# Kernel optimization log

Measured on AMD Instinct MI355X. Metric: run time of the kernel, lower is better.

## Reference

```python
import jax, jax.numpy as jnp
import numpy as np

N_NODES = 100000
N_FEATURES = 512
N_HIDDEN = 256
N_EDGES = 3200000


def setup_inputs() -> dict:
    key = jax.random.key(0)
    k_x, k_r, k_c, k_v, k_w, k_b = jax.random.split(key, 6)
    x = jax.random.normal(k_x, (1, N_NODES, N_FEATURES), dtype=jnp.float32)
    adj_rows = jax.random.randint(k_r, (N_EDGES,), 0, N_NODES, dtype=jnp.int32)
    adj_cols = jax.random.randint(k_c, (N_EDGES,), 0, N_NODES, dtype=jnp.int32)
    adj_vals = jax.random.uniform(k_v, (N_EDGES,), dtype=jnp.float32)
    # Linear params: xavier_normal_ on weight [H, F], default bias init
    std = float(np.sqrt(2.0 / (N_FEATURES + N_HIDDEN)))
    W = jax.random.normal(k_w, (N_HIDDEN, N_FEATURES), dtype=jnp.float32) * std
    bound = float(1.0 / np.sqrt(N_FEATURES))
    b = jax.random.uniform(k_b, (N_HIDDEN,), dtype=jnp.float32, minval=-bound, maxval=bound)
    alpha = jnp.asarray(0.25, dtype=jnp.float32)  # PReLU default single-param init
    return {"x": x, "adj_rows": adj_rows, "adj_cols": adj_cols,
            "adj_vals": adj_vals, "W": W, "b": b, "alpha": alpha}


def reference(x, adj_rows, adj_cols, adj_vals, W, b, alpha):
    # Linear: [1, N, F] @ [F, H] + [H] -> squeeze to [N, H]
    h = (jnp.einsum('bnf,hf->bnh', x, W) + b)[0]
    # spmm(adj, h): gather source rows, scale by edge value, scatter-add to dest rows
    msgs = adj_vals[:, None] * h[adj_cols]              # [E, H]
    agg = jax.ops.segment_sum(msgs, adj_rows, num_segments=N_NODES)  # [N, H]
    out = jnp.where(agg >= 0, agg, alpha * agg)         # PReLU
    return out[None]                                     # [1, N, H]
```

## Files before the change

### kernel.cpp

```cpp
#include <hip/hip_runtime.h>


#define K_DIM 512
#define H_DIM 256

#define BIN_ROWS 512
#define NBIN_MAX 256
#define EB 18432
#define P1_CHUNK 4096
#define P1_PER_T 4
#define SPU 8

typedef __attribute__((ext_vector_type(8))) short short8;
typedef __attribute__((ext_vector_type(4))) float floatx4;

__device__ inline short f32_to_bf16(float f) {
    unsigned u = __float_as_uint(f);
    u += 0x7fffu + ((u >> 16) & 1u);
    return (short)(u >> 16);
}
__device__ inline float bf16_to_f32(unsigned short u) {
    return __uint_as_float(((unsigned)u) << 16);
}

__global__ __launch_bounds__(256) void convert_w_kernel(
    const float* __restrict__ W, unsigned short* __restrict__ Wbf)
{
    int i = (blockIdx.x * 256 + threadIdx.x) * 8;
    float4 a = *(const float4*)(W + i);
    float4 b = *(const float4*)(W + i + 4);
    short8 v;
    v[0] = f32_to_bf16(a.x); v[1] = f32_to_bf16(a.y);
    v[2] = f32_to_bf16(a.z); v[3] = f32_to_bf16(a.w);
    v[4] = f32_to_bf16(b.x); v[5] = f32_to_bf16(b.y);
    v[6] = f32_to_bf16(b.z); v[7] = f32_to_bf16(b.w);
    *(short8*)((short*)Wbf + i) = v;
}

#define GT_M 128
#define GT_N 256
#define GT_K 32
#define LDSW 32

__global__ __launch_bounds__(256, 2) void gemm_bf16_kernel(
    const float* __restrict__ A,
    const unsigned short* __restrict__ Wbf,
    const float* __restrict__ bias,
    unsigned short* __restrict__ H,
    int M)
{
    __shared__ short As[GT_M * LDSW];
    __shared__ short Bs[GT_N * LDSW];

    const int tid  = threadIdx.x;
    const int m0   = blockIdx.x * GT_M;

    const int wave = tid >> 6;
    const int lane = tid & 63;
    const int wm   = (wave & 1) * 64;
    const int wn   = (wave >> 1) * 128;
    const int quad = lane >> 4;
    const int l16  = lane & 15;

    const int srow  = tid >> 1;
    const int shalf = tid & 1;

    floatx4 acc[4][8] = {};

    for (int k0 = 0; k0 < K_DIM; k0 += GT_K) {
        {
            int gm = m0 + srow;
            float f[16];
            if (gm < M) {
                const float* src = A + (size_t)gm * K_DIM + k0 + shalf * 16;
                *(float4*)(f + 0)  = *(const float4*)(src + 0);
                *(float4*)(f + 4)  = *(const float4*)(src + 4);
                *(float4*)(f + 8)  = *(const float4*)(src + 8);
                *(float4*)(f + 12) = *(const float4*)(src + 12);
            } else {
                #pragma unroll
                for (int j = 0; j < 16; ++j) f[j] = 0.f;
            }
            short8 v0, v1;
            #pragma unroll
            for (int j = 0; j < 8; ++j) { v0[j] = f32_to_bf16(f[j]); v1[j] = f32_to_bf16(f[8 + j]); }
            *(short8*)&As[srow * LDSW + shalf * 16 + 0] = v0;
            *(short8*)&As[srow * LDSW + shalf * 16 + 8] = v1;
        }
        #pragma unroll
        for (int it = 0; it < 2; ++it) {
            int gn = srow + it * 128;
            const unsigned short* src = Wbf + (size_t)gn * K_DIM + k0 + shalf * 16;
            short8 v0 = *(const short8*)(src + 0);
            short8 v1 = *(const short8*)(src + 8);
            *(short8*)&Bs[gn * LDSW + shalf * 16 + 0] = v0;
            *(short8*)&Bs[gn * LDSW + shalf * 16 + 8] = v1;
        }
        __syncthreads();

        short8 af[4], bf[8];
        #pragma unroll
        for (int t = 0; t < 4; ++t)
            af[t] = *(const short8*)&As[(wm + t * 16 + l16) * LDSW + quad * 8];
        #pragma unroll
        for (int t = 0; t < 8; ++t)
            bf[t] = *(const short8*)&Bs[(wn + t * 16 + l16) * LDSW + quad * 8];
        #pragma unroll
        for (int i = 0; i < 4; ++i)
            #pragma unroll
            for (int j = 0; j < 8; ++j)
                acc[i][j] = __builtin_amdgcn_mfma_f32_16x16x32_bf16(af[i], bf[j], acc[i][j], 0, 0, 0);
        __syncthreads();
    }

    #pragma unroll
    for (int j = 0; j < 8; ++j) {
        int gcol = wn + j * 16 + l16;
        float bj = bias[gcol];
        #pragma unroll
        for (int i = 0; i < 4; ++i) {
            int rbase = m0 + wm + i * 16 + quad * 4;
            #pragma unroll
            for (int r = 0; r < 4; ++r) {
                int gm = rbase + r;
                if (gm < M)
                    H[(size_t)gm * H_DIM + gcol] =
                        (unsigned short)f32_to_bf16(acc[i][j][r] + bj);
            }
        }
    }
}

__global__ __launch_bounds__(1024) void partition_kernel(
    const int* __restrict__ rows, const int* __restrict__ cols,
    const float* __restrict__ vals, int* __restrict__ binCursor,
    int2* __restrict__ binned, int E, int nbins)
{
    __shared__ int hist[NBIN_MAX];
    __shared__ int binOff[NBIN_MAX];
    __shared__ int gbase[NBIN_MAX];
    __shared__ int cursor[NBIN_MAX];
    __shared__ int sc[2][NBIN_MAX];
    __shared__ int2 stage[P1_CHUNK];
    __shared__ unsigned char binOf[P1_CHUNK];

    const int tid = threadIdx.x;
    const int e0  = blockIdx.x * P1_CHUNK;
    const int total = min(P1_CHUNK, E - e0);

    int r[P1_PER_T], c[P1_PER_T];
    float v[P1_PER_T];
    #pragma unroll
    for (int i = 0; i < P1_PER_T; ++i) {
        int e = e0 + tid + i * 1024;
        if (e < E) { r[i] = rows[e]; c[i] = cols[e]; v[i] = vals[e]; }
        else       { r[i] = -1; c[i] = 0; v[i] = 0.f; }
    }

    if (tid < NBIN_MAX) hist[tid] = 0;
    __syncthreads();
    #pragma unroll
    for (int i = 0; i < P1_PER_T; ++i)
        if (r[i] >= 0) atomicAdd(&hist[r[i] >> 9], 1);
    __syncthreads();

    if (tid < NBIN_MAX) sc[0][tid] = hist[tid];
    __syncthreads();
    int cur = 0;
    for (int d = 1; d < NBIN_MAX; d <<= 1) {
        if (tid < NBIN_MAX) {
            int y = sc[cur][tid];
            if (tid >= d) y += sc[cur][tid - d];
            sc[cur ^ 1][tid] = y;
        }
        __syncthreads();
        cur ^= 1;
    }
    if (tid < NBIN_MAX) {
        int x    = hist[tid];
        int excl = sc[cur][tid] - x;
        binOff[tid] = excl;
        cursor[tid] = excl;
        if (tid < nbins) gbase[tid] = atomicAdd(&binCursor[tid], x);
        else             gbase[tid] = 0;
    }
    __syncthreads();

    #pragma unroll
    for (int i = 0; i < P1_PER_T; ++i) {
        if (r[i] >= 0) {
            int bin  = r[i] >> 9;
            int lpos = atomicAdd(&cursor[bin], 1);
            stage[lpos] = make_int2(((r[i] & (BIN_ROWS - 1)) << 17) | c[i],
                                    __float_as_int(v[i]));
            binOf[lpos] = (unsigned char)bin;
        }
    }
    __syncthreads();

    #pragma unroll
    for (int i = 0; i < P1_PER_T; ++i) {
        int idx = tid + i * 1024;
        if (idx < total) {
            int bin = binOf[idx];
            int rel = gbase[bin] + (idx - binOff[bin]);
            if (rel < EB)
                binned[(size_t)bin * EB + rel] = stage[idx];
        }
    }
}

__global__ __launch_bounds__(1024) void binsort_kernel(
    const int2* __restrict__ binned, const int* __restrict__ binCursor,
    int2* __restrict__ sorted, int* __restrict__ rowstart,
    int* __restrict__ degArr, int M)
{
    __shared__ int hist[BIN_ROWS];
    __shared__ int cursor[BIN_ROWS];
    __shared__ int sc[2][BIN_ROWS];

    const int b   = blockIdx.x;
    const int tid = threadIdx.x;
    int cnt = binCursor[b]; if (cnt > EB) cnt = EB;
    int rows_here = M - b * BIN_ROWS; if (rows_here > BIN_ROWS) rows_here = BIN_ROWS;

    if (tid < BIN_ROWS) hist[tid] = 0;
    __syncthreads();
    const int2* src = binned + (size_t)b * EB;
    for (int i = tid; i < cnt; i += 1024)
        atomicAdd(&hist[((unsigned)src[i].x) >> 17], 1);
    __syncthreads();

    if (tid < BIN_ROWS) sc[0][tid] = hist[tid];
    __syncthreads();
    int cur = 0;
    for (int d = 1; d < BIN_ROWS; d <<= 1) {
        if (tid < BIN_ROWS) {
            int y = sc[cur][tid];
            if (tid >= d) y += sc[cur][tid - d];
            sc[cur ^ 1][tid] = y;
        }
        __syncthreads();
        cur ^= 1;
    }
    if (tid < BIN_ROWS) {
        int x    = hist[tid];
        int excl = sc[cur][tid] - x;
        cursor[tid] = excl;
        if (tid < rows_here) {
            rowstart[b * BIN_ROWS + tid] = b * EB + excl;
            degArr[b * BIN_ROWS + tid]   = x;
        }
    }
    __syncthreads();

    int2* dst = sorted + (size_t)b * EB;
    for (int i = tid; i < cnt; i += 1024) {
        int2 p  = src[i];
        int rl  = ((unsigned)p.x) >> 17;
        int pos = atomicAdd(&cursor[rl], 1);
        dst[pos] = make_int2(p.x & 0x1FFFF, p.y);
    }
}

__global__ __launch_bounds__(256) void spmm_gather_kernel(
    const unsigned short* __restrict__ h, const int* __restrict__ rowstart,
    const int* __restrict__ degArr, const int2* __restrict__ sorted,
    const float* __restrict__ alpha_p, float* __restrict__ out, int M)
{
    const int wave = threadIdx.x >> 6;
    const int lane = threadIdx.x & 63;
    const int row = blockIdx.x * 4 + wave;
    if (row >= M) return;

    const int deg = degArr[row];
    const int2* ep = sorted + rowstart[row];

    float4 acc = make_float4(0.f, 0.f, 0.f, 0.f);

    for (int chunk = 0; chunk < deg; chunk += 64) {
        int rem = deg - chunk;
        int n   = rem < 64 ? rem : 64;
        int ru  = (n + SPU - 1) & ~(SPU - 1);
        int2 p  = (chunk + lane < deg) ? ep[chunk + lane] : make_int2(0, 0);

        ushort4 u[SPU]; float vv[SPU];
        #pragma unroll
        for (int j = 0; j < SPU; ++j) {
            int c  = __shfl(p.x, j);
            vv[j]  = __int_as_float(__shfl(p.y, j));
            u[j]   = *(const ushort4*)(h + (size_t)c * H_DIM + lane * 4);
        }
        for (int e = SPU; e < ru; e += SPU) {
            ushort4 u2[SPU]; float vv2[SPU];
            #pragma unroll
            for (int j = 0; j < SPU; ++j) {
                int c   = __shfl(p.x, e + j);
                vv2[j]  = __int_as_float(__shfl(p.y, e + j));
                u2[j]   = *(const ushort4*)(h + (size_t)c * H_DIM + lane * 4);
            }
            #pragma unroll
            for (int j = 0; j < SPU; ++j) {
                float v = vv[j];
                acc.x += v * bf16_to_f32(u[j].x);
                acc.y += v * bf16_to_f32(u[j].y);
                acc.z += v * bf16_to_f32(u[j].z);
                acc.w += v * bf16_to_f32(u[j].w);
            }
            #pragma unroll
            for (int j = 0; j < SPU; ++j) { u[j] = u2[j]; vv[j] = vv2[j]; }
        }
        #pragma unroll
        for (int j = 0; j < SPU; ++j) {
            float v = vv[j];
            acc.x += v * bf16_to_f32(u[j].x);
            acc.y += v * bf16_to_f32(u[j].y);
            acc.z += v * bf16_to_f32(u[j].z);
            acc.w += v * bf16_to_f32(u[j].w);
        }
    }

    const float alpha = *alpha_p;
    acc.x = acc.x >= 0.f ? acc.x : alpha * acc.x;
    acc.y = acc.y >= 0.f ? acc.y : alpha * acc.y;
    acc.z = acc.z >= 0.f ? acc.z : alpha * acc.z;
    acc.w = acc.w >= 0.f ? acc.w : alpha * acc.w;
    *(float4*)(out + (size_t)row * H_DIM + lane * 4) = acc;
}

extern "C" void kernel_launch(void* const* d_in, const int* in_sizes, int n_in,
                              void* d_out, int out_size, void* d_ws, size_t ws_size,
                              hipStream_t stream) {
    const float* x        = (const float*)d_in[0];
    const int*   adj_rows = (const int*)d_in[1];
    const int*   adj_cols = (const int*)d_in[2];
    const float* adj_vals = (const float*)d_in[3];
    const float* W        = (const float*)d_in[4];
    const float* b        = (const float*)d_in[5];
    const float* alpha    = (const float*)d_in[6];
    float* out = (float*)d_out;

    const int M = in_sizes[0] / K_DIM;
    const int E = in_sizes[1];
    const int nbins = (M + BIN_ROWS - 1) / BIN_ROWS;

    char* ws = (char*)d_ws;
    size_t off = 0;
    auto alloc = [&](size_t bytes) {
        char* p = ws + off;
        off += (bytes + 255) & ~(size_t)255;
        return p;
    };
    unsigned short* h = (unsigned short*)alloc((size_t)M * H_DIM * sizeof(unsigned short));
    int2* binned  = (int2*)alloc((size_t)nbins * EB * sizeof(int2));
    int2* sorted  = (int2*)alloc((size_t)nbins * EB * sizeof(int2));
    int*  rowstart = (int*)alloc((size_t)M * sizeof(int));
    int*  degArr   = (int*)alloc((size_t)M * sizeof(int));
    int*  binCursor = (int*)alloc((size_t)NBIN_MAX * sizeof(int));
    unsigned short* Wbf = (unsigned short*)alloc((size_t)H_DIM * K_DIM * sizeof(unsigned short));

    convert_w_kernel<<<64, 256, 0, stream>>>(W, Wbf);

    gemm_bf16_kernel<<<dim3((M + GT_M - 1) / GT_M, 1), 256, 0, stream>>>(x, Wbf, b, h, M);

    hipMemsetAsync(binCursor, 0, (size_t)NBIN_MAX * sizeof(int), stream);
    partition_kernel<<<(E + P1_CHUNK - 1) / P1_CHUNK, 1024, 0, stream>>>(
        adj_rows, adj_cols, adj_vals, binCursor, binned, E, nbins);

    binsort_kernel<<<nbins, 1024, 0, stream>>>(binned, binCursor, sorted,
                                               rowstart, degArr, M);

    spmm_gather_kernel<<<(M + 3) / 4, 256, 0, stream>>>(h, rowstart, degArr, sorted,
                                                        alpha, out, M);
}
```

Before: 652.1 us.

## Restructure GEMM: 512-thread blocks, W fragments from global, register-prefetched A

The GEMM now runs 8 waves per block, each owning a 64x64 output tile instead of 64x128. The shared-memory staging of W is removed, so each wave reads its bf16 W fragments directly from global (L2-resident) memory. The next A slice is prefetched into registers while the current slice is computed. This cuts LDS footprint and per-wave register use to raise occupancy and overlap the fp32 x loads with MFMA work, at the cost of redundant global W reads across waves and blocks.

After: 664.3 us. About the same (+1.9%).

```diff
diff --git a/kernel.cpp b/kernel.cpp
--- a/kernel.cpp
+++ b/kernel.cpp
@@ -38,11 +38,11 @@
 }
 
 #define GT_M 128
-#define GT_N 256
 #define GT_K 32
+#define NSTEP (K_DIM / GT_K)
 #define LDSW 32
 
-__global__ __launch_bounds__(256, 2) void gemm_bf16_kernel(
+__global__ __launch_bounds__(512, 4) void gemm_bf16_kernel(
     const float* __restrict__ A,
     const unsigned short* __restrict__ Wbf,
     const float* __restrict__ bias,
@@ -50,71 +50,68 @@
     int M)
 {
     __shared__ short As[GT_M * LDSW];
-    __shared__ short Bs[GT_N * LDSW];
 
     const int tid  = threadIdx.x;
     const int m0   = blockIdx.x * GT_M;
 
     const int wave = tid >> 6;
     const int lane = tid & 63;
-    const int wm   = (wave & 1) * 64;
-    const int wn   = (wave >> 1) * 128;
+    const int wm   = (wave >> 2) * 64;
+    const int wn   = (wave & 3) * 64;
     const int quad = lane >> 4;
     const int l16  = lane & 15;
 
-    const int srow  = tid >> 1;
-    const int shalf = tid & 1;
-
-    floatx4 acc[4][8] = {};
-
-    for (int k0 = 0; k0 < K_DIM; k0 += GT_K) {
-        {
-            int gm = m0 + srow;
-            float f[16];
-            if (gm < M) {
-                const float* src = A + (size_t)gm * K_DIM + k0 + shalf * 16;
-                *(float4*)(f + 0)  = *(const float4*)(src + 0);
-                *(float4*)(f + 4)  = *(const float4*)(src + 4);
-                *(float4*)(f + 8)  = *(const float4*)(src + 8);
-                *(float4*)(f + 12) = *(const float4*)(src + 12);
-            } else {
-                #pragma unroll
-                for (int j = 0; j < 16; ++j) f[j] = 0.f;
-            }
-            short8 v0, v1;
-            #pragma unroll
-            for (int j = 0; j < 8; ++j) { v0[j] = f32_to_bf16(f[j]); v1[j] = f32_to_bf16(f[8 + j]); }
-            *(short8*)&As[srow * LDSW + shalf * 16 + 0] = v0;
-            *(short8*)&As[srow * LDSW + shalf * 16 + 8] = v1;
-        }
-        #pragma unroll
-        for (int it = 0; it < 2; ++it) {
-            int gn = srow + it * 128;
-            const unsigned short* src = Wbf + (size_t)gn * K_DIM + k0 + shalf * 16;
-            short8 v0 = *(const short8*)(src + 0);
-            short8 v1 = *(const short8*)(src + 8);
-            *(short8*)&Bs[gn * LDSW + shalf * 16 + 0] = v0;
-            *(short8*)&Bs[gn * LDSW + shalf * 16 + 8] = v1;
-        }
+    const int arow  = tid >> 2;
+    const int apart = tid & 3;
+
+    floatx4 acc[4][4] = {};
+
+    const bool arow_ok = (m0 + arow) < M;
+    const float* asrc = A + (size_t)(m0 + arow) * K_DIM + apart * 8;
+
+    float f[8];
+    if (arow_ok) {
+        *(float4*)(f + 0) = *(const float4*)(asrc + 0);
+        *(float4*)(f + 4) = *(const float4*)(asrc + 4);
+    } else {
+        #pragma unroll
+        for (int j = 0; j < 8; ++j) f[j] = 0.f;
+    }
+
+    for (int ks = 0; ks < NSTEP; ++ks) {
+        short8 v;
+        #pragma unroll
+        for (int j = 0; j < 8; ++j) v[j] = f32_to_bf16(f[j]);
+        *(short8*)&As[arow * LDSW + apart * 8] = v;
         __syncthreads();
 
-        short8 af[4], bf[8];
+        if (ks + 1 < NSTEP && arow_ok) {
+            const float* s2 = asrc + (ks + 1) * GT_K;
+            *(float4*)(f + 0) = *(const float4*)(s2 + 0);
+            *(float4*)(f + 4) = *(const float4*)(s2 + 4);
+        }
+
+        short8 bf[4];
+        const int kb = ks * GT_K + quad * 8;
+        #pragma unroll
+        for (int t = 0; t < 4; ++t)
+            bf[t] = *(const short8*)(Wbf + (size_t)(wn + t * 16 + l16) * K_DIM + kb);
+
+        short8 af[4];
         #pragma unroll
         for (int t = 0; t < 4; ++t)
             af[t] = *(const short8*)&As[(wm + t * 16 + l16) * LDSW + quad * 8];
-        #pragma unroll
-        for (int t = 0; t < 8; ++t)
-            bf[t] = *(const short8*)&Bs[(wn + t * 16 + l16) * LDSW + quad * 8];
+
         #pragma unroll
         for (int i = 0; i < 4; ++i)
             #pragma unroll
-            for (int j = 0; j < 8; ++j)
+            for (int j = 0; j < 4; ++j)
                 acc[i][j] = __builtin_amdgcn_mfma_f32_16x16x32_bf16(af[i], bf[j], acc[i][j], 0, 0, 0);
         __syncthreads();
     }
 
     #pragma unroll
-    for (int j = 0; j < 8; ++j) {
+    for (int j = 0; j < 4; ++j) {
         int gcol = wn + j * 16 + l16;
         float bj = bias[gcol];
         #pragma unroll
@@ -361,7 +358,7 @@
 
     convert_w_kernel<<<64, 256, 0, stream>>>(W, Wbf);
 
-    gemm_bf16_kernel<<<dim3((M + GT_M - 1) / GT_M, 1), 256, 0, stream>>>(x, Wbf, b, h, M);
+    gemm_bf16_kernel<<<dim3((M + GT_M - 1) / GT_M, 1), 512, 0, stream>>>(x, Wbf, b, h, M);
 
     hipMemsetAsync(binCursor, 0, (size_t)NBIN_MAX * sizeof(int), stream);
     partition_kernel<<<(E + P1_CHUNK - 1) / P1_CHUNK, 1024, 0, stream>>>(
```
